# Kernel optimization log

Hardware: AMD Instinct MI355X
Metric: run time of the kernel (lower is better)

The kernel has to match this reference:

```python
import jax, jax.numpy as jnp
import numpy as np

N = 100000   # nodes
E = 3200000  # edges (avg degree 32)
NFEAT, NHID, NCLASS = 256, 128, 16


def setup_inputs() -> dict:
    key = jax.random.key(0)
    ks = jax.random.split(key, 8)
    x = jax.random.normal(ks[0], (N, NFEAT), dtype=jnp.float32)
    W1 = jax.random.normal(ks[1], (NFEAT, NHID), dtype=jnp.float32) / np.sqrt(NFEAT)
    b1 = jnp.zeros((NHID,), dtype=jnp.float32)
    W2 = jax.random.normal(ks[2], (NHID, NCLASS), dtype=jnp.float32) / np.sqrt(NHID)
    b2 = jnp.zeros((NCLASS,), dtype=jnp.float32)
    edge_weight = jax.random.uniform(ks[3], (E,), dtype=jnp.float32)
    src = jax.random.randint(ks[4], (E,), 0, N, dtype=jnp.int32)
    dst = jax.random.randint(ks[5], (E,), 0, N, dtype=jnp.int32)
    return {"x": x, "W1": W1, "b1": b1, "W2": W2, "b2": b2,
            "edge_weight": edge_weight, "src": src, "dst": dst}


def _spmm(edge_weight, src, dst, h):
    # adj @ h with adj given as COO edge list: out[dst] += w * h[src]
    msgs = edge_weight[:, None] * h[src]            # [E, d]
    return jax.ops.segment_sum(msgs, dst, num_segments=N)


def reference(x, W1, b1, W2, b2, edge_weight, src, dst):
    # gc1: spmm(adj, x @ W1) + b1, then relu (dropout is identity in eval)
    h = _spmm(edge_weight, src, dst, x @ W1) + b1   # [N, NHID]
    h = jax.nn.relu(h)
    # gc2: spmm(adj, h @ W2) + b2
    logits = _spmm(edge_weight, src, dst, h @ W2) + b2  # [N, NCLASS]
    return jax.nn.log_softmax(logits, axis=1)
```

## Files before the change

### kernel.cpp

```cpp
#include <hip/hip_runtime.h>

#define NN 100000
#define EE 3200000
#define NF 256
#define NH 128
#define NC 16
#define NBKT 391
#define BSZ 256
#define BCAP 9600
#define CHUNK 4096

typedef __bf16 bf16;
typedef bf16 bf16x2 __attribute__((ext_vector_type(2)));
typedef bf16 bf16x4 __attribute__((ext_vector_type(4)));
typedef bf16 bf16x8 __attribute__((ext_vector_type(8)));
typedef float f32x2 __attribute__((ext_vector_type(2)));
typedef float f32x4 __attribute__((ext_vector_type(4)));


__global__ void k_init(int* __restrict__ bucket_cursor, int2* __restrict__ edges) {
    int t = threadIdx.x;
    if (t < NBKT) bucket_cursor[t] = t * BCAP;
    if (t >= 496) edges[EE + t - 496] = make_int2(0, 0);
}

__global__ __launch_bounds__(512) void k_bucket(const int* __restrict__ src,
                                                const int* __restrict__ dst,
                                                const float* __restrict__ ew,
                                                int* __restrict__ bucket_cursor,
                                                int2* __restrict__ staged) {
    __shared__ int2 recs[CHUNK];
    __shared__ unsigned short bkt[CHUNK];
    __shared__ int cnt[NBKT], start[NBKT + 1], cur[NBKT], gbase[NBKT];
    __shared__ int sc[512];
    int t = threadIdx.x;
    int base = blockIdx.x * CHUNK;
    int n = EE - base; if (n > CHUNK) n = CHUNK;
    if (t < NBKT) cnt[t] = 0;
    __syncthreads();
    for (int i = t; i < n; i += 512) {
        atomicAdd(&cnt[dst[base + i] >> 8], 1);
    }
    __syncthreads();
    sc[t] = (t < NBKT) ? cnt[t] : 0;
    __syncthreads();
    for (int off = 1; off < 512; off <<= 1) {
        int v = (t >= off) ? sc[t - off] : 0;
        __syncthreads();
        sc[t] += v;
        __syncthreads();
    }
    if (t < NBKT) { start[t] = sc[t] - cnt[t]; cur[t] = sc[t] - cnt[t]; }
    if (t == 0) start[NBKT] = sc[511];
    __syncthreads();
    for (int i = t; i < n; i += 512) {
        int d = dst[base + i];
        int b = d >> 8;
        int p = atomicAdd(&cur[b], 1);
        recs[p] = make_int2(src[base + i] | ((d & 255) << 17), __float_as_int(ew[base + i]));
        bkt[p] = (unsigned short)b;
    }
    __syncthreads();
    if (t < NBKT) gbase[t] = atomicAdd(&bucket_cursor[t], start[t + 1] - start[t]);
    __syncthreads();
    for (int i = t; i < n; i += 512) {
        int b = bkt[i];
        staged[gbase[b] + (i - start[b])] = recs[i];
    }
}

__global__ void k_bscan(const int* __restrict__ bucket_cursor,
                        int* __restrict__ bucket_base, int* __restrict__ row_off) {
    __shared__ int s[512];
    int t = threadIdx.x;
    int v = (t < NBKT) ? (bucket_cursor[t] - t * BCAP) : 0;
    s[t] = v;
    __syncthreads();
    for (int off = 1; off < 512; off <<= 1) {
        int x = (t >= off) ? s[t - off] : 0;
        __syncthreads();
        s[t] += x;
        __syncthreads();
    }
    if (t < NBKT) bucket_base[t] = s[t] - v;
    if (t == 0) { bucket_base[NBKT] = EE; row_off[NN] = EE; }
}

__global__ __launch_bounds__(512) void k_sort(const int2* __restrict__ staged,
                                              const int* __restrict__ bucket_cursor,
                                              const int* __restrict__ bucket_base,
                                              int* __restrict__ row_off,
                                              int2* __restrict__ edges) {
    __shared__ int2 lrec[BCAP];
    __shared__ int lcnt[BSZ], lstart[BSZ], lcur[BSZ];
    int t = threadIdx.x;
    int b = blockIdx.x;
    int n = bucket_cursor[b] - b * BCAP;
    int gb = bucket_base[b];
    const int2* sp = staged + (size_t)b * BCAP;
    if (t < BSZ) lcnt[t] = 0;
    __syncthreads();
    for (int i = t; i < n; i += 512) {
        int2 r = sp[i];
        lrec[i] = r;
        atomicAdd(&lcnt[r.x >> 17], 1);
    }
    __syncthreads();
    if (t < BSZ) lstart[t] = lcnt[t];
    __syncthreads();
    for (int off = 1; off < BSZ; off <<= 1) {
        int v = 0;
        if (t < BSZ && t >= off) v = lstart[t - off];
        __syncthreads();
        if (t < BSZ) lstart[t] += v;
        __syncthreads();
    }
    if (t < BSZ) {
        int ex = lstart[t] - lcnt[t];
        lcur[t] = ex;
        int node = (b << 8) + t;
        if (node < NN) row_off[node] = gb + ex;
    }
    __syncthreads();
    for (int i = t; i < n; i += 512) {
        int2 r = lrec[i];
        int d = r.x >> 17;
        int p = atomicAdd(&lcur[d], 1);
        edges[gb + p] = make_int2(r.x & 0x1FFFF, r.y);
    }
}


__global__ void k_cvtW1(const float* __restrict__ W1, bf16* __restrict__ W1T) {
    int i = blockIdx.x * 256 + threadIdx.x;
    int k = i >> 7, n = i & 127;
    W1T[n * NF + k] = (bf16)W1[i];
}

__global__ __launch_bounds__(256, 2) void k_gemm1(const float* __restrict__ x,
                                                  const bf16* __restrict__ W1T,
                                                  unsigned char* __restrict__ h0q) {
    __shared__ unsigned short sW[NH * NF];
    int t = threadIdx.x;
    int lane = t & 63;
    int wid = t >> 6;
    int m = lane & 15;
    int kg = lane >> 4;
    int rowbase = blockIdx.x * 128 + wid * 32;

    bf16x8 a[2][8];
#pragma unroll
    for (int tile = 0; tile < 2; tile++) {
        int row = rowbase + tile * 16 + m;
        bool in = (row < NN);
        const float* xr = x + (size_t)row * NF;
#pragma unroll
        for (int kt = 0; kt < 8; kt++) {
            int k0 = kt * 32 + kg * 8;
            float4 u = in ? *(const float4*)(xr + k0)     : make_float4(0.f, 0.f, 0.f, 0.f);
            float4 v = in ? *(const float4*)(xr + k0 + 4) : make_float4(0.f, 0.f, 0.f, 0.f);
            bf16x8 av = { (bf16)u.x, (bf16)u.y, (bf16)u.z, (bf16)u.w,
                          (bf16)v.x, (bf16)v.y, (bf16)v.z, (bf16)v.w };
            a[tile][kt] = av;
        }
    }

    for (int cid = t; cid < NH * (NF / 8); cid += 256) {
        int n = cid >> 5, ch = cid & 31;
        bf16x8 v = *(const bf16x8*)(W1T + (size_t)n * NF + ch * 8);
        *(bf16x8*)&sW[n * NF + ((ch ^ (n & 7)) << 3)] = v;
    }
    __syncthreads();

    f32x4 acc[2][8] = {};
#pragma unroll
    for (int ct = 0; ct < 8; ct++) {
        int brow = ct * 16 + m;
        const unsigned short* bp = sW + brow * NF;
        int sw = brow & 7;
#pragma unroll
        for (int kt = 0; kt < 8; kt++) {
            int ch = kt * 4 + kg;
            bf16x8 b = *(const bf16x8*)(bp + ((ch ^ sw) << 3));
            acc[0][ct] = __builtin_amdgcn_mfma_f32_16x16x32_bf16(a[0][kt], b, acc[0][ct], 0, 0, 0);
            acc[1][ct] = __builtin_amdgcn_mfma_f32_16x16x32_bf16(a[1][kt], b, acc[1][ct], 0, 0, 0);
        }
    }

#pragma unroll
    for (int tile = 0; tile < 2; tile++) {
        int rbase = rowbase + tile * 16 + kg * 4;
#pragma unroll
        for (int ct = 0; ct < 8; ct++) {
            int col = ct * 16 + m;
#pragma unroll
            for (int r = 0; r < 4; r++) {
                int rr = rbase + r;
                if (rr < NN) {
                    unsigned px = (unsigned)__builtin_amdgcn_cvt_pk_fp8_f32(
                                      acc[tile][ct][r], acc[tile][ct][r], 0, false);
                    h0q[(size_t)rr * NH + col] = (unsigned char)(px & 0xffu);
                }
            }
        }
    }
}


__global__ __launch_bounds__(256) void k_spmm1(const int* __restrict__ row_off,
                                               const int2* __restrict__ edges,
                                               const unsigned char* __restrict__ h0q,
                                               const float* __restrict__ b1,
                                               bf16* __restrict__ h) {
    int wid = __builtin_amdgcn_readfirstlane(threadIdx.x >> 6);
    int node = blockIdx.x * 4 + wid;
    int lane = threadIdx.x & 63;
    int lq = lane & 31;
    bool hhi = lane >= 32;
    int s = row_off[node], e = row_off[node + 1];

    unsigned loff = (unsigned)lq * 4u;

    float a0[2] = {0.f, 0.f}, a1[2] = {0.f, 0.f};
    float a2[2] = {0.f, 0.f}, a3[2] = {0.f, 0.f};

    for (int i = s; i < e; i += 16) {
        int2 q[16];
#pragma unroll
        for (int j = 0; j < 16; j++) q[j] = edges[i + j];
        unsigned so[8]; float wo[8];
#pragma unroll
        for (int j = 0; j < 8; j++) {
            bool v0 = (i + 2 * j)     < e;
            bool v1 = (i + 2 * j + 1) < e;
            unsigned s0 = v0 ? (unsigned)q[2 * j].x : 0u;
            unsigned s1 = v1 ? (unsigned)q[2 * j + 1].x : 0u;
            float w0 = v0 ? __int_as_float(q[2 * j].y) : 0.f;
            float w1 = v1 ? __int_as_float(q[2 * j + 1].y) : 0.f;
            so[j] = hhi ? s1 : s0;
            wo[j] = hhi ? w1 : w0;
        }
        unsigned dv[8];
#pragma unroll
        for (int j = 0; j < 8; j++) {
            unsigned off = (so[j] << 7) + loff;
            dv[j] = *(const unsigned*)(h0q + off);
        }
#pragma unroll
        for (int j = 0; j < 8; j++) {
            f32x2 f01 = __builtin_amdgcn_cvt_pk_f32_fp8(dv[j], false);
            f32x2 f23 = __builtin_amdgcn_cvt_pk_f32_fp8(dv[j], true);
            int p = j & 1;
            a0[p] += wo[j] * f01[0];
            a1[p] += wo[j] * f01[1];
            a2[p] += wo[j] * f23[0];
            a3[p] += wo[j] * f23[1];
        }
    }
    float t0 = a0[0] + a0[1];
    float t1 = a1[0] + a1[1];
    float t2 = a2[0] + a2[1];
    float t3 = a3[0] + a3[1];
    t0 += __shfl_xor(t0, 32);
    t1 += __shfl_xor(t1, 32);
    t2 += __shfl_xor(t2, 32);
    t3 += __shfl_xor(t3, 32);
    if (!hhi) {
        float4 bv = ((const float4*)b1)[lq];
        float r0 = fmaxf(t0 + bv.x, 0.f);
        float r1 = fmaxf(t1 + bv.y, 0.f);
        float r2 = fmaxf(t2 + bv.z, 0.f);
        float r3 = fmaxf(t3 + bv.w, 0.f);
        bf16x4 o = { (bf16)r0, (bf16)r1, (bf16)r2, (bf16)r3 };
        *(bf16x4*)(h + (size_t)node * NH + lq * 4) = o;
    }
}


__global__ __launch_bounds__(256) void k_gemm2(const bf16* __restrict__ h,
                                               const float* __restrict__ W2,
                                               bf16* __restrict__ g) {
    __shared__ float sW[NH * NC];
    int t = threadIdx.x;
    for (int i = t; i < NH * NC; i += 256) sW[i] = W2[i];
    __syncthreads();
    int row = blockIdx.x * 256 + t;
    if (row >= NN) return;
    const bf16* hr = h + (size_t)row * NH;
    float acc[NC] = {};
    for (int kc = 0; kc < NH / 8; kc++) {
        bf16x8 hv = *(const bf16x8*)(hr + kc * 8);
#pragma unroll
        for (int j = 0; j < 8; j++) {
            float hx = (float)hv[j];
            const float* wr = &sW[(kc * 8 + j) * NC];
#pragma unroll
            for (int c = 0; c < NC; c++) acc[c] += hx * wr[c];
        }
    }
    bf16x8 o0 = { (bf16)acc[0], (bf16)acc[1], (bf16)acc[2],  (bf16)acc[3],
                  (bf16)acc[4], (bf16)acc[5], (bf16)acc[6],  (bf16)acc[7] };
    bf16x8 o1 = { (bf16)acc[8], (bf16)acc[9], (bf16)acc[10], (bf16)acc[11],
                  (bf16)acc[12], (bf16)acc[13], (bf16)acc[14], (bf16)acc[15] };
    bf16* gr = g + (size_t)row * NC;
    *(bf16x8*)gr = o0;
    *(bf16x8*)(gr + 8) = o1;
}


__global__ __launch_bounds__(256) void k_spmm2(const int* __restrict__ row_off,
                                               const int2* __restrict__ edges,
                                               const bf16* __restrict__ g,
                                               const float* __restrict__ b2,
                                               float* __restrict__ out) {
    int node = (blockIdx.x * 256 + threadIdx.x) >> 6;
    int lane = threadIdx.x & 63;
    int c = lane & 15, sub = lane >> 4;
    int s = row_off[node], e = row_off[node + 1];
    const unsigned short* gbp = (const unsigned short*)g;

    float acc[4] = { 0.f, 0.f, 0.f, 0.f };
    for (int i = s + sub; i < e; i += 16) {
        unsigned sx[4]; float w[4];
#pragma unroll
        for (int k = 0; k < 4; k++) {
            int idx = i + 4 * k;
            int2 r = edges[idx];
            bool v = idx < e;
            sx[k] = v ? (unsigned)r.x : 0u;
            w[k]  = v ? __int_as_float(r.y) : 0.f;
        }
#pragma unroll
        for (int k = 0; k < 4; k++) {
            unsigned hv = gbp[sx[k] * NC + c];
            acc[k] += w[k] * __int_as_float(hv << 16);
        }
    }
    float a = (acc[0] + acc[1]) + (acc[2] + acc[3]);
    a += __shfl_xor(a, 16);
    a += __shfl_xor(a, 32);
    a += b2[c];
    float m = a;
#pragma unroll
    for (int off = 1; off < 16; off <<= 1) m = fmaxf(m, __shfl_xor(m, off));
    float ex = __expf(a - m);
    float sum = ex;
#pragma unroll
    for (int off = 1; off < 16; off <<= 1) sum += __shfl_xor(sum, off);
    float r = a - m - __logf(sum);
    if (sub == 0) out[(size_t)node * NC + c] = r;
}


extern "C" void kernel_launch(void* const* d_in, const int* in_sizes, int n_in,
                              void* d_out, int out_size, void* d_ws, size_t ws_size,
                              hipStream_t stream) {
    const float* x  = (const float*)d_in[0];
    const float* W1 = (const float*)d_in[1];
    const float* b1 = (const float*)d_in[2];
    const float* W2 = (const float*)d_in[3];
    const float* b2 = (const float*)d_in[4];
    const float* ew = (const float*)d_in[5];
    const int* src  = (const int*)d_in[6];
    const int* dst  = (const int*)d_in[7];
    float* out = (float*)d_out;

    char* ws = (char*)d_ws;
    unsigned char* h0q = (unsigned char*)(ws + 0);
    bf16*  h       = (bf16*)(ws + 25600000);
    bf16*  g       = (bf16*)(ws + 51200000);
    int*   row_off = (int*)(ws + 54400000);
    int*   bucket_cursor = (int*)(ws + 54800016);
    int*   bucket_base   = (int*)(ws + 54801584);
    int2*  edges   = (int2*)(ws + 54803168);
    bf16*  W1T     = (bf16*)(ws + 80403296);
    int2*  staged  = (int2*)(ws + 0);

    k_init<<<1, 512, 0, stream>>>(bucket_cursor, edges);
    k_bucket<<<(EE + CHUNK - 1) / CHUNK, 512, 0, stream>>>(src, dst, ew, bucket_cursor, staged);
    k_bscan<<<1, 512, 0, stream>>>(bucket_cursor, bucket_base, row_off);
    k_sort<<<NBKT, 512, 0, stream>>>(staged, bucket_cursor, bucket_base, row_off, edges);

    k_cvtW1<<<(NF * NH) / 256, 256, 0, stream>>>(W1, W1T);
    k_gemm1<<<(NN + 127) / 128, 256, 0, stream>>>(x, W1T, h0q);
    k_spmm1<<<NN / 4, 256, 0, stream>>>(row_off, edges, h0q, b1, h);

    k_gemm2<<<(NN + 255) / 256, 256, 0, stream>>>(h, W2, g);
    k_spmm2<<<NN / 4, 256, 0, stream>>>(row_off, edges, g, b2, out);
}
```

Measured before the change: 399.1 us.

## Restructure gemm1 to one tile per wave with packed fp8 stores; unroll spmm1 wider

```diff
diff --git a/kernel.cpp b/kernel.cpp
--- a/kernel.cpp
+++ b/kernel.cpp
@@ -21,7 +21,7 @@
 __global__ void k_init(int* __restrict__ bucket_cursor, int2* __restrict__ edges) {
     int t = threadIdx.x;
     if (t < NBKT) bucket_cursor[t] = t * BCAP;
-    if (t >= 496) edges[EE + t - 496] = make_int2(0, 0);
+    if (t >= 480) edges[EE + t - 480] = make_int2(0, 0);
 }
 
 __global__ __launch_bounds__(512) void k_bucket(const int* __restrict__ src,
@@ -137,7 +137,7 @@
     W1T[n * NF + k] = (bf16)W1[i];
 }
 
-__global__ __launch_bounds__(256, 2) void k_gemm1(const float* __restrict__ x,
+__global__ __launch_bounds__(512, 4) void k_gemm1(const float* __restrict__ x,
                                                   const bf16* __restrict__ W1T,
                                                   unsigned char* __restrict__ h0q) {
     __shared__ unsigned short sW[NH * NF];
@@ -146,33 +146,29 @@
     int wid = t >> 6;
     int m = lane & 15;
     int kg = lane >> 4;
-    int rowbase = blockIdx.x * 128 + wid * 32;
-
-    bf16x8 a[2][8];
-#pragma unroll
-    for (int tile = 0; tile < 2; tile++) {
-        int row = rowbase + tile * 16 + m;
-        bool in = (row < NN);
-        const float* xr = x + (size_t)row * NF;
-#pragma unroll
-        for (int kt = 0; kt < 8; kt++) {
-            int k0 = kt * 32 + kg * 8;
-            float4 u = in ? *(const float4*)(xr + k0)     : make_float4(0.f, 0.f, 0.f, 0.f);
-            float4 v = in ? *(const float4*)(xr + k0 + 4) : make_float4(0.f, 0.f, 0.f, 0.f);
-            bf16x8 av = { (bf16)u.x, (bf16)u.y, (bf16)u.z, (bf16)u.w,
-                          (bf16)v.x, (bf16)v.y, (bf16)v.z, (bf16)v.w };
-            a[tile][kt] = av;
-        }
-    }
-
-    for (int cid = t; cid < NH * (NF / 8); cid += 256) {
+    int row = blockIdx.x * 128 + wid * 16 + m;
+    bool in = (row < NN);
+    const float* xr = x + (size_t)row * NF;
+
+    bf16x8 a[8];
+#pragma unroll
+    for (int kt = 0; kt < 8; kt++) {
+        int k0 = kt * 32 + kg * 8;
+        float4 u = in ? *(const float4*)(xr + k0)     : make_float4(0.f, 0.f, 0.f, 0.f);
+        float4 v = in ? *(const float4*)(xr + k0 + 4) : make_float4(0.f, 0.f, 0.f, 0.f);
+        bf16x8 av = { (bf16)u.x, (bf16)u.y, (bf16)u.z, (bf16)u.w,
+                      (bf16)v.x, (bf16)v.y, (bf16)v.z, (bf16)v.w };
+        a[kt] = av;
+    }
+
+    for (int cid = t; cid < NH * (NF / 8); cid += 512) {
         int n = cid >> 5, ch = cid & 31;
         bf16x8 v = *(const bf16x8*)(W1T + (size_t)n * NF + ch * 8);
         *(bf16x8*)&sW[n * NF + ((ch ^ (n & 7)) << 3)] = v;
     }
     __syncthreads();
 
-    f32x4 acc[2][8] = {};
+    f32x4 acc[8] = {};
 #pragma unroll
     for (int ct = 0; ct < 8; ct++) {
         int brow = ct * 16 + m;
@@ -182,26 +178,19 @@
         for (int kt = 0; kt < 8; kt++) {
             int ch = kt * 4 + kg;
             bf16x8 b = *(const bf16x8*)(bp + ((ch ^ sw) << 3));
-            acc[0][ct] = __builtin_amdgcn_mfma_f32_16x16x32_bf16(a[0][kt], b, acc[0][ct], 0, 0, 0);
-            acc[1][ct] = __builtin_amdgcn_mfma_f32_16x16x32_bf16(a[1][kt], b, acc[1][ct], 0, 0, 0);
-        }
-    }
-
-#pragma unroll
-    for (int tile = 0; tile < 2; tile++) {
-        int rbase = rowbase + tile * 16 + kg * 4;
+            acc[ct] = __builtin_amdgcn_mfma_f32_16x16x32_bf16(b, a[kt], acc[ct], 0, 0, 0);
+        }
+    }
+
+    if (in) {
+        unsigned char* rp = h0q + (size_t)row * NH + kg * 4;
 #pragma unroll
         for (int ct = 0; ct < 8; ct++) {
-            int col = ct * 16 + m;
-#pragma unroll
-            for (int r = 0; r < 4; r++) {
-                int rr = rbase + r;
-                if (rr < NN) {
-                    unsigned px = (unsigned)__builtin_amdgcn_cvt_pk_fp8_f32(
-                                      acc[tile][ct][r], acc[tile][ct][r], 0, false);
-                    h0q[(size_t)rr * NH + col] = (unsigned char)(px & 0xffu);
-                }
-            }
+            unsigned lo = (unsigned)__builtin_amdgcn_cvt_pk_fp8_f32(
+                              acc[ct][0], acc[ct][1], 0, false);
+            unsigned pk = (unsigned)__builtin_amdgcn_cvt_pk_fp8_f32(
+                              acc[ct][2], acc[ct][3], lo, true);
+            *(unsigned*)(rp + ct * 16) = pk;
         }
     }
 }
@@ -224,13 +213,13 @@
     float a0[2] = {0.f, 0.f}, a1[2] = {0.f, 0.f};
     float a2[2] = {0.f, 0.f}, a3[2] = {0.f, 0.f};
 
-    for (int i = s; i < e; i += 16) {
-        int2 q[16];
-#pragma unroll
-        for (int j = 0; j < 16; j++) q[j] = edges[i + j];
-        unsigned so[8]; float wo[8];
-#pragma unroll
-        for (int j = 0; j < 8; j++) {
+    for (int i = s; i < e; i += 32) {
+        int2 q[32];
+#pragma unroll
+        for (int j = 0; j < 32; j++) q[j] = edges[i + j];
+        unsigned so[16]; float wo[16];
+#pragma unroll
+        for (int j = 0; j < 16; j++) {
             bool v0 = (i + 2 * j)     < e;
             bool v1 = (i + 2 * j + 1) < e;
             unsigned s0 = v0 ? (unsigned)q[2 * j].x : 0u;
@@ -240,14 +229,14 @@
             so[j] = hhi ? s1 : s0;
             wo[j] = hhi ? w1 : w0;
         }
-        unsigned dv[8];
-#pragma unroll
-        for (int j = 0; j < 8; j++) {
+        unsigned dv[16];
+#pragma unroll
+        for (int j = 0; j < 16; j++) {
             unsigned off = (so[j] << 7) + loff;
             dv[j] = *(const unsigned*)(h0q + off);
         }
 #pragma unroll
-        for (int j = 0; j < 8; j++) {
+        for (int j = 0; j < 16; j++) {
             f32x2 f01 = __builtin_amdgcn_cvt_pk_f32_fp8(dv[j], false);
             f32x2 f23 = __builtin_amdgcn_cvt_pk_f32_fp8(dv[j], true);
             int p = j & 1;
@@ -373,7 +362,7 @@
     int*   bucket_cursor = (int*)(ws + 54800016);
     int*   bucket_base   = (int*)(ws + 54801584);
     int2*  edges   = (int2*)(ws + 54803168);
-    bf16*  W1T     = (bf16*)(ws + 80403296);
+    bf16*  W1T     = (bf16*)(ws + 80403456);
     int2*  staged  = (int2*)(ws + 0);
 
     k_init<<<1, 512, 0, stream>>>(bucket_cursor, edges);
@@ -382,7 +371,7 @@
     k_sort<<<NBKT, 512, 0, stream>>>(staged, bucket_cursor, bucket_base, row_off, edges);
 
     k_cvtW1<<<(NF * NH) / 256, 256, 0, stream>>>(W1, W1T);
-    k_gemm1<<<(NN + 127) / 128, 256, 0, stream>>>(x, W1T, h0q);
+    k_gemm1<<<(NN + 127) / 128, 512, 0, stream>>>(x, W1T, h0q);
     k_spmm1<<<NN / 4, 256, 0, stream>>>(row_off, edges, h0q, b1, h);
 
     k_gemm2<<<(NN + 255) / 256, 256, 0, stream>>>(h, W2, g);
```

Measured after the change: 408.2 us. 2.3% more time.
